# Optimization experiments

Measured on AMD Instinct MI355X. Metric: run time of the kernel, lower is better.

The kernel has to match this reference:

```python
import jax, jax.numpy as jnp
import numpy as np

B, T, C, H = 4, 2048, 1024, 16
HD = C // H
SCALE = 1.0 / np.sqrt(HD).astype(np.float32)


def setup_inputs() -> dict:
    key = jax.random.key(0)
    k1, k2, k3, k4 = jax.random.split(key, 4)
    x = jax.random.normal(k1, (B, T, C), dtype=jnp.float32)
    keys = jax.random.normal(k2, (B, T, C), dtype=jnp.float32)
    queries = jax.random.normal(k3, (B, T, C), dtype=jnp.float32)
    mask = jnp.ones((B, T), dtype=jnp.float32)
    Wp = jax.random.normal(k4, (C, C), dtype=jnp.float32) * (1.0 / np.sqrt(C))
    bp = jnp.zeros((C,), dtype=jnp.float32)
    return {"x": x, "keys": keys, "queries": queries, "mask": mask, "Wp": Wp, "bp": bp}


def reference(x, keys, queries, mask, Wp, bp):
    Bc, Tc, Cc = x.shape
    # [B,T,C] -> [B,H,T,hd]
    def split_heads(t):
        return t.reshape(Bc, Tc, H, HD).transpose(0, 2, 1, 3)

    m = mask[:, None, :, None]  # [B,1,T,1]
    q = split_heads(queries) * m
    k = split_heads(keys) * m
    v = split_heads(x) * m
    # no softmax: linear bilinear attention; dropout=0 (eval) is identity
    att = jnp.einsum('bhqd,bhkd->bhqk', q, k) * SCALE  # [B,H,T,T]
    y = jnp.einsum('bhqk,bhkd->bhqd', att, v)          # [B,H,T,hd]
    y = y.transpose(0, 2, 1, 3).reshape(Bc, Tc, Cc)
    y = y @ Wp.T + bp  # torch Linear: x W^T + b
    return (y, att)
```

## Files before the change

### kernel.cpp

```cpp
#include <hip/hip_runtime.h>

#define Bdim 4
#define T 2048
#define C 1024
#define H 16
#define HD 64
#define SCALE 0.125f

typedef __attribute__((ext_vector_type(8))) short short8;
typedef __attribute__((ext_vector_type(4))) float f32x4;

__device__ inline unsigned short f2bf(float f) {
  unsigned int u = __float_as_uint(f);
  return (unsigned short)((u + 0x7FFFu + ((u >> 16) & 1u)) >> 16);
}
__device__ inline float bf2f(unsigned short s) {
  return __uint_as_float(((unsigned int)s) << 16);
}

#define OFF_QS   (0)
#define OFF_KS   (16u*1024u*1024u)
#define OFF_WPB  (32u*1024u*1024u)
#define OFF_PART (34u*1024u*1024u)
#define OFF_KTV  (38u*1024u*1024u)
#define OFF_YPRE (39u*1024u*1024u)

__global__ __launch_bounds__(256) void k_convert_qk(
    const float* __restrict__ queries, const float* __restrict__ keys,
    const float* __restrict__ mask,
    unsigned short* __restrict__ Qs, unsigned short* __restrict__ Ks) {
  int idx = blockIdx.x * 256 + threadIdx.x;
  long e = (long)idx * 8;
  int b = (int)(e / ((long)T * C));
  int rem = (int)(e % ((long)T * C));
  int t = rem / C;
  int c = rem % C;
  int h = c >> 6, d = c & 63;
  float m = mask[b * T + t];
  const float4* qp = (const float4*)(queries + e);
  const float4* kp = (const float4*)(keys + e);
  float4 q0 = qp[0], q1 = qp[1];
  float4 k0 = kp[0], k1 = kp[1];
  float qv[8] = {q0.x,q0.y,q0.z,q0.w,q1.x,q1.y,q1.z,q1.w};
  float kv[8] = {k0.x,k0.y,k0.z,k0.w,k1.x,k1.y,k1.z,k1.w};
  unsigned short qo[8], ko[8];
  #pragma unroll
  for (int j = 0; j < 8; ++j) {
    qo[j] = f2bf(qv[j] * m * SCALE);
    ko[j] = f2bf(kv[j] * m);
  }
  long dst = ((long)(b * H + h) * T + t) * HD + d;
  *(short8*)(Qs + dst) = *(const short8*)qo;
  *(short8*)(Ks + dst) = *(const short8*)ko;
}

__global__ __launch_bounds__(256) void k_convert_wp(
    const float* __restrict__ Wp, unsigned short* __restrict__ Wpb) {
  long e = ((long)blockIdx.x * 256 + threadIdx.x) * 8;
  const float4* wp = (const float4*)(Wp + e);
  float4 w0 = wp[0], w1 = wp[1];
  float wv[8] = {w0.x,w0.y,w0.z,w0.w,w1.x,w1.y,w1.z,w1.w};
  unsigned short wo[8];
  #pragma unroll
  for (int j = 0; j < 8; ++j) wo[j] = f2bf(wv[j]);
  *(short8*)(Wpb + e) = *(const short8*)wo;
}

__global__ __launch_bounds__(256) void k_att(
    const unsigned short* __restrict__ Qs, const unsigned short* __restrict__ Ks,
    float* __restrict__ att) {
  int bid = blockIdx.x;
  int wg = ((bid & 7) << 11) | (bid >> 3);
  int bh = wg >> 8;
  int tile = wg & 255;
  int tm = tile >> 4, tn = tile & 15;
  int tid = threadIdx.x;
  int lane = tid & 63, wid = tid >> 6;
  int wr = wid >> 1, wc = wid & 1;
  int lr = lane & 15, kg = lane >> 4;
  const unsigned short* Q = Qs + (long)bh * T * HD;
  const unsigned short* K = Ks + (long)bh * T * HD;
  int row0 = tm * 128 + wr * 64;
  int col0 = tn * 128 + wc * 64;
  short8 a[4][2], b[4][2];
  #pragma unroll
  for (int i = 0; i < 4; ++i) {
    #pragma unroll
    for (int kk = 0; kk < 2; ++kk) {
      a[i][kk] = *(const short8*)(Q + (long)(row0 + i*16 + lr)*HD + kk*32 + kg*8);
      b[i][kk] = *(const short8*)(K + (long)(col0 + i*16 + lr)*HD + kk*32 + kg*8);
    }
  }
  f32x4 acc[4][4];
  #pragma unroll
  for (int i = 0; i < 4; ++i)
    #pragma unroll
    for (int j = 0; j < 4; ++j)
      acc[i][j] = (f32x4){0.f, 0.f, 0.f, 0.f};
  #pragma unroll
  for (int i = 0; i < 4; ++i) {
    #pragma unroll
    for (int j = 0; j < 4; ++j) {
      acc[i][j] = __builtin_amdgcn_mfma_f32_16x16x32_bf16(a[i][0], b[j][0], acc[i][j], 0, 0, 0);
      acc[i][j] = __builtin_amdgcn_mfma_f32_16x16x32_bf16(a[i][1], b[j][1], acc[i][j], 0, 0, 0);
    }
  }
  float* ob = att + (long)bh * T * T;
  #pragma unroll
  for (int i = 0; i < 4; ++i) {
    #pragma unroll
    for (int r = 0; r < 4; ++r) {
      int row = row0 + i*16 + kg*4 + r;
      float* orow = ob + (long)row * T + col0 + lr;
      #pragma unroll
      for (int j = 0; j < 4; ++j) orow[j*16] = acc[i][j][r];
    }
  }
}

__global__ __launch_bounds__(256) void k_ktv_partial(
    const float* __restrict__ keys, const float* __restrict__ x,
    const float* __restrict__ mask, float* __restrict__ part) {
  int bid = blockIdx.x;
  int bh = bid >> 2, p = bid & 3;
  int b = bh >> 4, h = bh & 15;
  __shared__ float ks[16][64];
  __shared__ float vs[16][64];
  int tid = threadIdx.x;
  int ty = tid >> 4, tx = tid & 15;
  float acc[4][4];
  #pragma unroll
  for (int i = 0; i < 4; ++i)
    #pragma unroll
    for (int j = 0; j < 4; ++j) acc[i][j] = 0.f;
  int tbeg = p * 512;
  for (int t0 = tbeg; t0 < tbeg + 512; t0 += 16) {
    __syncthreads();
    for (int e = tid; e < 1024; e += 256) {
      int tt = e >> 6, d = e & 63;
      long gi = ((long)(b * T + t0 + tt)) * C + h * 64 + d;
      float m = mask[b * T + t0 + tt];
      ks[tt][d] = keys[gi] * m;
      vs[tt][d] = x[gi] * m;
    }
    __syncthreads();
    #pragma unroll 4
    for (int tt = 0; tt < 16; ++tt) {
      float ka[4], va[4];
      #pragma unroll
      for (int i = 0; i < 4; ++i) { ka[i] = ks[tt][ty + 16*i]; va[i] = vs[tt][tx + 16*i]; }
      #pragma unroll
      for (int i = 0; i < 4; ++i)
        #pragma unroll
        for (int j = 0; j < 4; ++j) acc[i][j] += ka[i] * va[j];
    }
  }
  float* o = part + (long)bid * 4096;
  #pragma unroll
  for (int i = 0; i < 4; ++i)
    #pragma unroll
    for (int j = 0; j < 4; ++j) o[(ty + 16*i) * 64 + tx + 16*j] = acc[i][j];
}

__global__ __launch_bounds__(256) void k_ktv_reduce(
    const float* __restrict__ part, float* __restrict__ ktv) {
  int i = blockIdx.x * 256 + threadIdx.x;
  int bh = i >> 12, off = i & 4095;
  const float* pp = part + (long)bh * 4 * 4096 + off;
  ktv[i] = pp[0] + pp[4096] + pp[8192] + pp[12288];
}

__global__ __launch_bounds__(256) void k_ypre(
    const unsigned short* __restrict__ Qs, const float* __restrict__ ktv,
    unsigned short* __restrict__ ypre) {
  int blk = blockIdx.x;
  int b = blk >> 7;
  int t0 = (blk & 127) << 4;
  __shared__ float qsm[16][68];
  __shared__ float kv[64][64];
  int tid = threadIdx.x;
  int rown = tid >> 4;
  int c0 = (tid & 15) * 4;
  for (int h = 0; h < H; ++h) {
    __syncthreads();
    const unsigned short* qh = Qs + ((long)(b * H + h) * T + t0) * HD;
    for (int e = tid; e < 1024; e += 256) qsm[e >> 6][e & 63] = bf2f(qh[(e >> 6) * HD + (e & 63)]);
    const float* kh = ktv + (b * H + h) * 4096;
    for (int e = tid; e < 4096; e += 256) kv[e >> 6][e & 63] = kh[e];
    __syncthreads();
    float a0 = 0.f, a1 = 0.f, a2 = 0.f, a3 = 0.f;
    #pragma unroll 8
    for (int d1 = 0; d1 < 64; ++d1) {
      float q = qsm[rown][d1];
      a0 += q * kv[d1][c0 + 0];
      a1 += q * kv[d1][c0 + 1];
      a2 += q * kv[d1][c0 + 2];
      a3 += q * kv[d1][c0 + 3];
    }
    unsigned short* yo = ypre + ((long)(b * T + t0 + rown)) * C + h * HD + c0;
    yo[0] = f2bf(a0); yo[1] = f2bf(a1); yo[2] = f2bf(a2); yo[3] = f2bf(a3);
  }
}

__global__ __launch_bounds__(256) void k_proj(
    const unsigned short* __restrict__ A, const unsigned short* __restrict__ Bw,
    const float* __restrict__ bp, float* __restrict__ y) {
  int bid = blockIdx.x;
  int wg = ((bid & 7) << 6) | (bid >> 3);
  int tm = wg >> 3, tn = wg & 7;
  int tid = threadIdx.x;
  int lane = tid & 63, wid = tid >> 6;
  int wr = wid >> 1, wc = wid & 1;
  int lr = lane & 15, kg = lane >> 4;
  int row0 = tm * 128 + wr * 64;
  int col0 = tn * 128 + wc * 64;
  f32x4 acc[4][4];
  #pragma unroll
  for (int i = 0; i < 4; ++i)
    #pragma unroll
    for (int j = 0; j < 4; ++j) acc[i][j] = (f32x4){0.f, 0.f, 0.f, 0.f};
  #pragma unroll 4
  for (int k0 = 0; k0 < C; k0 += 32) {
    short8 av[4], bv[4];
    #pragma unroll
    for (int i = 0; i < 4; ++i)
      av[i] = *(const short8*)(A + (long)(row0 + i*16 + lr) * C + k0 + kg*8);
    #pragma unroll
    for (int j = 0; j < 4; ++j)
      bv[j] = *(const short8*)(Bw + (long)(col0 + j*16 + lr) * C + k0 + kg*8);
    #pragma unroll
    for (int i = 0; i < 4; ++i)
      #pragma unroll
      for (int j = 0; j < 4; ++j)
        acc[i][j] = __builtin_amdgcn_mfma_f32_16x16x32_bf16(av[i], bv[j], acc[i][j], 0, 0, 0);
  }
  #pragma unroll
  for (int i = 0; i < 4; ++i) {
    #pragma unroll
    for (int r = 0; r < 4; ++r) {
      int row = row0 + i*16 + kg*4 + r;
      float* orow = y + (long)row * C;
      #pragma unroll
      for (int j = 0; j < 4; ++j) {
        int col = col0 + j*16 + lr;
        orow[col] = acc[i][j][r] + bp[col];
      }
    }
  }
}

extern "C" void kernel_launch(void* const* d_in, const int* in_sizes, int n_in,
                              void* d_out, int out_size, void* d_ws, size_t ws_size,
                              hipStream_t stream) {
  const float* x       = (const float*)d_in[0];
  const float* keys    = (const float*)d_in[1];
  const float* queries = (const float*)d_in[2];
  const float* mask    = (const float*)d_in[3];
  const float* Wp      = (const float*)d_in[4];
  const float* bp      = (const float*)d_in[5];

  float* y   = (float*)d_out;
  float* att = (float*)d_out + (long)Bdim * T * C;

  char* ws = (char*)d_ws;
  unsigned short* Qs   = (unsigned short*)(ws + OFF_QS);
  unsigned short* Ks   = (unsigned short*)(ws + OFF_KS);
  unsigned short* Wpb  = (unsigned short*)(ws + OFF_WPB);
  float* part          = (float*)(ws + OFF_PART);
  float* ktv           = (float*)(ws + OFF_KTV);
  unsigned short* ypre = (unsigned short*)(ws + OFF_YPRE);

  k_convert_qk<<<dim3(4096), dim3(256), 0, stream>>>(queries, keys, mask, Qs, Ks);
  k_convert_wp<<<dim3(512), dim3(256), 0, stream>>>(Wp, Wpb);
  k_att<<<dim3(16384), dim3(256), 0, stream>>>(Qs, Ks, att);
  k_ktv_partial<<<dim3(256), dim3(256), 0, stream>>>(keys, x, mask, part);
  k_ktv_reduce<<<dim3(1024), dim3(256), 0, stream>>>(part, ktv);
  k_ypre<<<dim3(512), dim3(256), 0, stream>>>(Qs, ktv, ypre);
  k_proj<<<dim3(512), dim3(256), 0, stream>>>(ypre, Wpb, bp, y);
}
```

Measured before the change: 502.8 us.

## Fold K^T V into projection weights and vectorize attention stores

Replaces the ypre kernel and the separate Wp conversion with a per-batch folded weight G = (K^T V per head) times Wp^T, so the output becomes a single GEMM of Q against G. The att kernel swaps MFMA operands so each lane holds four contiguous columns, and writes them as nontemporal 16-byte stores instead of scalar strided stores. The K^T V partial split is doubled to 8 chunks for more parallelism. This adds a per-batch 1024x1024 bf16 G buffer and changes where the rounding to bf16 happens.

```diff
diff --git a/kernel.cpp b/kernel.cpp
--- a/kernel.cpp
+++ b/kernel.cpp
@@ -14,16 +14,12 @@
   unsigned int u = __float_as_uint(f);
   return (unsigned short)((u + 0x7FFFu + ((u >> 16) & 1u)) >> 16);
 }
-__device__ inline float bf2f(unsigned short s) {
-  return __uint_as_float(((unsigned int)s) << 16);
-}
-
-#define OFF_QS   (0)
+
+#define OFF_QS   (0u)
 #define OFF_KS   (16u*1024u*1024u)
-#define OFF_WPB  (32u*1024u*1024u)
-#define OFF_PART (34u*1024u*1024u)
-#define OFF_KTV  (38u*1024u*1024u)
-#define OFF_YPRE (39u*1024u*1024u)
+#define OFF_PART (32u*1024u*1024u)
+#define OFF_KTV  (40u*1024u*1024u)
+#define OFF_GT   (41u*1024u*1024u)
 
 __global__ __launch_bounds__(256) void k_convert_qk(
     const float* __restrict__ queries, const float* __restrict__ keys,
@@ -54,18 +50,6 @@
   *(short8*)(Ks + dst) = *(const short8*)ko;
 }
 
-__global__ __launch_bounds__(256) void k_convert_wp(
-    const float* __restrict__ Wp, unsigned short* __restrict__ Wpb) {
-  long e = ((long)blockIdx.x * 256 + threadIdx.x) * 8;
-  const float4* wp = (const float4*)(Wp + e);
-  float4 w0 = wp[0], w1 = wp[1];
-  float wv[8] = {w0.x,w0.y,w0.z,w0.w,w1.x,w1.y,w1.z,w1.w};
-  unsigned short wo[8];
-  #pragma unroll
-  for (int j = 0; j < 8; ++j) wo[j] = f2bf(wv[j]);
-  *(short8*)(Wpb + e) = *(const short8*)wo;
-}
-
 __global__ __launch_bounds__(256) void k_att(
     const unsigned short* __restrict__ Qs, const unsigned short* __restrict__ Ks,
     float* __restrict__ att) {
@@ -101,19 +85,17 @@
   for (int i = 0; i < 4; ++i) {
     #pragma unroll
     for (int j = 0; j < 4; ++j) {
-      acc[i][j] = __builtin_amdgcn_mfma_f32_16x16x32_bf16(a[i][0], b[j][0], acc[i][j], 0, 0, 0);
-      acc[i][j] = __builtin_amdgcn_mfma_f32_16x16x32_bf16(a[i][1], b[j][1], acc[i][j], 0, 0, 0);
+      acc[i][j] = __builtin_amdgcn_mfma_f32_16x16x32_bf16(b[j][0], a[i][0], acc[i][j], 0, 0, 0);
+      acc[i][j] = __builtin_amdgcn_mfma_f32_16x16x32_bf16(b[j][1], a[i][1], acc[i][j], 0, 0, 0);
     }
   }
   float* ob = att + (long)bh * T * T;
   #pragma unroll
   for (int i = 0; i < 4; ++i) {
-    #pragma unroll
-    for (int r = 0; r < 4; ++r) {
-      int row = row0 + i*16 + kg*4 + r;
-      float* orow = ob + (long)row * T + col0 + lr;
-      #pragma unroll
-      for (int j = 0; j < 4; ++j) orow[j*16] = acc[i][j][r];
+    long rbase = (long)(row0 + i*16 + lr) * T + col0 + kg*4;
+    #pragma unroll
+    for (int j = 0; j < 4; ++j) {
+      __builtin_nontemporal_store(acc[i][j], (f32x4*)(ob + rbase + j*16));
     }
   }
 }
@@ -122,7 +104,7 @@
     const float* __restrict__ keys, const float* __restrict__ x,
     const float* __restrict__ mask, float* __restrict__ part) {
   int bid = blockIdx.x;
-  int bh = bid >> 2, p = bid & 3;
+  int bh = bid >> 3, p = bid & 7;
   int b = bh >> 4, h = bh & 15;
   __shared__ float ks[16][64];
   __shared__ float vs[16][64];
@@ -133,8 +115,8 @@
   for (int i = 0; i < 4; ++i)
     #pragma unroll
     for (int j = 0; j < 4; ++j) acc[i][j] = 0.f;
-  int tbeg = p * 512;
-  for (int t0 = tbeg; t0 < tbeg + 512; t0 += 16) {
+  int tbeg = p * 256;
+  for (int t0 = tbeg; t0 < tbeg + 256; t0 += 16) {
     __syncthreads();
     for (int e = tid; e < 1024; e += 256) {
       int tt = e >> 6, d = e & 63;
@@ -166,48 +148,54 @@
     const float* __restrict__ part, float* __restrict__ ktv) {
   int i = blockIdx.x * 256 + threadIdx.x;
   int bh = i >> 12, off = i & 4095;
-  const float* pp = part + (long)bh * 4 * 4096 + off;
-  ktv[i] = pp[0] + pp[4096] + pp[8192] + pp[12288];
-}
-
-__global__ __launch_bounds__(256) void k_ypre(
-    const unsigned short* __restrict__ Qs, const float* __restrict__ ktv,
-    unsigned short* __restrict__ ypre) {
-  int blk = blockIdx.x;
-  int b = blk >> 7;
-  int t0 = (blk & 127) << 4;
-  __shared__ float qsm[16][68];
+  const float* pp = part + (long)bh * 8 * 4096 + off;
+  float s = 0.f;
+  #pragma unroll
+  for (int p = 0; p < 8; ++p) s += pp[p * 4096];
+  ktv[i] = s;
+}
+
+__global__ __launch_bounds__(256) void k_gt(
+    const float* __restrict__ ktv, const float* __restrict__ Wp,
+    unsigned short* __restrict__ Gt) {
+  int bid = blockIdx.x;
+  int b = bid >> 8;
+  int h = (bid >> 4) & 15;
+  int n0 = (bid & 15) * 64;
   __shared__ float kv[64][64];
-  int tid = threadIdx.x;
-  int rown = tid >> 4;
-  int c0 = (tid & 15) * 4;
-  for (int h = 0; h < H; ++h) {
-    __syncthreads();
-    const unsigned short* qh = Qs + ((long)(b * H + h) * T + t0) * HD;
-    for (int e = tid; e < 1024; e += 256) qsm[e >> 6][e & 63] = bf2f(qh[(e >> 6) * HD + (e & 63)]);
-    const float* kh = ktv + (b * H + h) * 4096;
-    for (int e = tid; e < 4096; e += 256) kv[e >> 6][e & 63] = kh[e];
-    __syncthreads();
-    float a0 = 0.f, a1 = 0.f, a2 = 0.f, a3 = 0.f;
-    #pragma unroll 8
-    for (int d1 = 0; d1 < 64; ++d1) {
-      float q = qsm[rown][d1];
-      a0 += q * kv[d1][c0 + 0];
-      a1 += q * kv[d1][c0 + 1];
-      a2 += q * kv[d1][c0 + 2];
-      a3 += q * kv[d1][c0 + 3];
-    }
-    unsigned short* yo = ypre + ((long)(b * T + t0 + rown)) * C + h * HD + c0;
-    yo[0] = f2bf(a0); yo[1] = f2bf(a1); yo[2] = f2bf(a2); yo[3] = f2bf(a3);
-  }
-}
-
-__global__ __launch_bounds__(256) void k_proj(
-    const unsigned short* __restrict__ A, const unsigned short* __restrict__ Bw,
+  __shared__ float wp[64][65];
+  int tid = threadIdx.x;
+  for (int e = tid; e < 4096; e += 256) {
+    kv[e >> 6][e & 63] = ktv[((b * H + h) << 12) + e];
+    wp[e >> 6][e & 63] = Wp[(long)(n0 + (e >> 6)) * C + h * 64 + (e & 63)];
+  }
+  __syncthreads();
+  int nl = tid & 63, dg = tid >> 6;
+  float s[16];
+  #pragma unroll
+  for (int dd = 0; dd < 16; ++dd) s[dd] = 0.f;
+  for (int e = 0; e < 64; ++e) {
+    float w = wp[nl][e];
+    #pragma unroll
+    for (int dd = 0; dd < 16; ++dd)
+      s[dd] += kv[dg * 16 + dd][e] * w;
+  }
+  unsigned short o[16];
+  #pragma unroll
+  for (int dd = 0; dd < 16; ++dd) o[dd] = f2bf(s[dd]);
+  unsigned short* dst = Gt + ((long)(b * C + n0 + nl)) * C + h * 64 + dg * 16;
+  *(short8*)dst = *(const short8*)o;
+  *(short8*)(dst + 8) = *(const short8*)(o + 8);
+}
+
+__global__ __launch_bounds__(256) void k_out(
+    const unsigned short* __restrict__ Qs, const unsigned short* __restrict__ Gt,
     const float* __restrict__ bp, float* __restrict__ y) {
   int bid = blockIdx.x;
   int wg = ((bid & 7) << 6) | (bid >> 3);
-  int tm = wg >> 3, tn = wg & 7;
+  int b = wg >> 7;
+  int tile = wg & 127;
+  int tm = tile >> 3, tn = tile & 7;
   int tid = threadIdx.x;
   int lane = tid & 63, wid = tid >> 6;
   int wr = wid >> 1, wc = wid & 1;
@@ -221,30 +209,32 @@
     for (int j = 0; j < 4; ++j) acc[i][j] = (f32x4){0.f, 0.f, 0.f, 0.f};
   #pragma unroll 4
   for (int k0 = 0; k0 < C; k0 += 32) {
+    int h = k0 >> 6;
+    int off = (k0 & 63) + kg * 8;
+    const unsigned short* qb = Qs + (long)(b * H + h) * T * HD;
+    const unsigned short* gb = Gt + (long)b * C * C + k0 + kg * 8;
     short8 av[4], bv[4];
     #pragma unroll
     for (int i = 0; i < 4; ++i)
-      av[i] = *(const short8*)(A + (long)(row0 + i*16 + lr) * C + k0 + kg*8);
+      av[i] = *(const short8*)(qb + (long)(row0 + i*16 + lr) * HD + off);
     #pragma unroll
     for (int j = 0; j < 4; ++j)
-      bv[j] = *(const short8*)(Bw + (long)(col0 + j*16 + lr) * C + k0 + kg*8);
+      bv[j] = *(const short8*)(gb + (long)(col0 + j*16 + lr) * C);
     #pragma unroll
     for (int i = 0; i < 4; ++i)
       #pragma unroll
       for (int j = 0; j < 4; ++j)
-        acc[i][j] = __builtin_amdgcn_mfma_f32_16x16x32_bf16(av[i], bv[j], acc[i][j], 0, 0, 0);
-  }
-  #pragma unroll
-  for (int i = 0; i < 4; ++i) {
-    #pragma unroll
-    for (int r = 0; r < 4; ++r) {
-      int row = row0 + i*16 + kg*4 + r;
-      float* orow = y + (long)row * C;
-      #pragma unroll
-      for (int j = 0; j < 4; ++j) {
-        int col = col0 + j*16 + lr;
-        orow[col] = acc[i][j][r] + bp[col];
-      }
+        acc[i][j] = __builtin_amdgcn_mfma_f32_16x16x32_bf16(bv[j], av[i], acc[i][j], 0, 0, 0);
+  }
+  #pragma unroll
+  for (int i = 0; i < 4; ++i) {
+    int row = row0 + i*16 + lr;
+    float* yrow = y + (long)(b * T + row) * C;
+    #pragma unroll
+    for (int j = 0; j < 4; ++j) {
+      int col = col0 + j*16 + kg*4;
+      f32x4 res = acc[i][j] + *(const f32x4*)(bp + col);
+      *(f32x4*)(yrow + col) = res;
     }
   }
 }
@@ -265,16 +255,14 @@
   char* ws = (char*)d_ws;
   unsigned short* Qs   = (unsigned short*)(ws + OFF_QS);
   unsigned short* Ks   = (unsigned short*)(ws + OFF_KS);
-  unsigned short* Wpb  = (unsigned short*)(ws + OFF_WPB);
   float* part          = (float*)(ws + OFF_PART);
   float* ktv           = (float*)(ws + OFF_KTV);
-  unsigned short* ypre = (unsigned short*)(ws + OFF_YPRE);
+  unsigned short* Gt   = (unsigned short*)(ws + OFF_GT);
 
   k_convert_qk<<<dim3(4096), dim3(256), 0, stream>>>(queries, keys, mask, Qs, Ks);
-  k_convert_wp<<<dim3(512), dim3(256), 0, stream>>>(Wp, Wpb);
+  k_ktv_partial<<<dim3(512), dim3(256), 0, stream>>>(keys, x, mask, part);
   k_att<<<dim3(16384), dim3(256), 0, stream>>>(Qs, Ks, att);
-  k_ktv_partial<<<dim3(256), dim3(256), 0, stream>>>(keys, x, mask, part);
   k_ktv_reduce<<<dim3(1024), dim3(256), 0, stream>>>(part, ktv);
-  k_ypre<<<dim3(512), dim3(256), 0, stream>>>(Qs, ktv, ypre);
-  k_proj<<<dim3(512), dim3(256), 0, stream>>>(ypre, Wpb, bp, y);
-}
+  k_gt<<<dim3(1024), dim3(256), 0, stream>>>(ktv, Wp, Gt);
+  k_out<<<dim3(512), dim3(256), 0, stream>>>(Qs, Gt, bp, y);
+}
```

After: 433.5 us. 1.16x faster.
